# Performance work log

Measured on AMD Instinct MI355X. Metric: run time of the kernel, lower is better.

The kernel has to match this reference:

```python
import jax, jax.numpy as jnp
import numpy as np

N, D, K, A, BINS, DEPTH = 1024, 384, 64, 5, 64, 4
D_MAX = 22.0


def _expected_distance(distogram):
    # distance_one_hot_inverse(softmax(distogram), 0.0, 22.0, 64)
    step = D_MAX / BINS
    centers = step * jnp.arange(BINS, dtype=distogram.dtype) + step / 2
    p = jax.nn.softmax(distogram, axis=-1)  # [N,N,BINS]
    return (p * centers).sum(axis=-1)       # [N,N]


def _extract_neighbours(pos, prev_pos, distogram, resi, chain, batch, mask, key):
    inf = jnp.inf
    same_batch = batch[:, None] == batch[None, :]
    same_chain = (chain[:, None] == chain[None, :]) & same_batch
    pair_mask = mask[:, None] & mask[None, :] & same_batch
    # sequence-separation distance (only within a chain), 3.81 A per residue
    seq_d = jnp.where(same_chain,
                      jnp.abs(resi[:, None] - resi[None, :]).astype(jnp.float32) * 3.81,
                      inf)
    md = _expected_distance(distogram)
    d = jnp.minimum(seq_d, jnp.where(md < 8.0, md, inf))
    ca = pos[:, 1]                                   # current CA positions [N,3]
    d = jnp.minimum(d, jnp.linalg.norm(ca[:, None] - ca[None, :], axis=-1))
    pca = prev_pos[:, 1]
    d = jnp.minimum(d, jnp.linalg.norm(pca[:, None] - pca[None, :], axis=-1))
    d = jnp.where(same_batch, d, inf)
    log_p = -3.0 * d
    u = jax.random.uniform(key, d.shape)
    gumbel = -jnp.log(-jnp.log(u + 1e-6) + 1e-6)
    random_distance = -(log_p + gumbel)
    random_distance = jnp.where(pair_mask, random_distance, inf)
    neg_vals, idx = jax.lax.top_k(-random_distance, K)  # k smallest random distances
    nbr_mask = jnp.isfinite(neg_vals)                   # invalid neighbours have -inf
    return idx, nbr_mask                                # [N,K] int32, [N,K] bool


def setup_inputs() -> dict:
    key = jax.random.key(0)
    ks = jax.random.split(key, 8)
    local = jax.random.normal(ks[0], (N, D), dtype=jnp.float32)
    pos = 3.0 * jax.random.normal(ks[1], (N, A, 3), dtype=jnp.float32)
    prev_pos = 3.0 * jax.random.normal(ks[2], (N, A, 3), dtype=jnp.float32)
    distogram = jax.random.normal(ks[3], (N, N, BINS), dtype=jnp.float32)
    Wn = jax.random.normal(ks[4], (D, D), dtype=jnp.float32) / np.sqrt(D)
    Wp = 0.01 * jax.random.normal(ks[5], (D, A * 3), dtype=jnp.float32)
    ar = jnp.arange(N, dtype=jnp.int32)
    batch = ar // 256          # 4 proteins of 256 residues
    chain = (ar // 128) % 2    # 2 chains per protein
    resi = ar % 128            # residue index within chain
    mask = jnp.ones((N,), dtype=bool)
    return {"local": local, "pos": pos, "prev_pos": prev_pos, "distogram": distogram,
            "Wn": Wn, "Wp": Wp, "resi": resi, "chain": chain, "batch": batch, "mask": mask}


def reference(local, pos, prev_pos, distogram, Wn, Wp, resi, chain, batch, mask):
    mask_f = mask.astype(local.dtype)
    key = jax.random.key(42)
    traj = []
    for t in range(DEPTH):  # diffusion_depth iterations, neighbours recomputed each block
        idx, nbr_mask = _extract_neighbours(pos, prev_pos, distogram, resi, chain,
                                            batch, mask, jax.random.fold_in(key, t))
        nf = local[idx] * nbr_mask[..., None].astype(local.dtype)   # [N,K,D]
        cnt = jnp.maximum(nbr_mask.sum(axis=1, keepdims=True).astype(local.dtype), 1.0)
        msg = nf.sum(axis=1) / cnt                                   # [N,D]
        local = local + jax.nn.gelu(msg @ Wn)
        pos = pos + 0.1 * (local @ Wp).reshape(N, A, 3) * mask_f[:, None, None]
        traj.append(pos)
    trajectory = jnp.stack(traj)  # [DEPTH,N,A,3]
    return local, pos, trajectory
```

## Files before the change

### kernel.cpp

```cpp
#include <hip/hip_runtime.h>
#include <stdint.h>

typedef unsigned int u32;
typedef unsigned long long u64;

#define NN 1024
#define DDIM 384
#define KNB 64
#define BINS_ 64
#define DEPTH_ 4

#define OUT_POS 393216
#define OUT_TRAJ 408576

__device__ __forceinline__ u32 rotl32(u32 x, int r) { return (x << r) | (x >> (32 - r)); }

__device__ __forceinline__ void threefry(u32 k0, u32 k1, u32 x0, u32 x1, u32& o0, u32& o1) {
  u32 ks2 = k0 ^ k1 ^ 0x1BD11BDAu;
#define TF_R(r) { x0 += x1; x1 = rotl32(x1, r); x1 ^= x0; }
  x0 += k0; x1 += k1;
  TF_R(13) TF_R(15) TF_R(26) TF_R(6)
  x0 += k1; x1 += ks2 + 1u;
  TF_R(17) TF_R(29) TF_R(16) TF_R(24)
  x0 += ks2; x1 += k0 + 2u;
  TF_R(13) TF_R(15) TF_R(26) TF_R(6)
  x0 += k0; x1 += k1 + 3u;
  TF_R(17) TF_R(29) TF_R(16) TF_R(24)
  x0 += k1; x1 += ks2 + 4u;
  TF_R(13) TF_R(15) TF_R(26) TF_R(6)
  x0 += ks2; x1 += k0 + 5u;
#undef TF_R
  o0 = x0; o1 = x1;
}

static inline u32 h_rotl32(u32 x, int r) { return (x << r) | (x >> (32 - r)); }
static void h_threefry(u32 k0, u32 k1, u32 x0, u32 x1, u32& o0, u32& o1) {
  u32 ks2 = k0 ^ k1 ^ 0x1BD11BDAu;
#define TF_R(r) { x0 += x1; x1 = h_rotl32(x1, r); x1 ^= x0; }
  x0 += k0; x1 += k1;
  TF_R(13) TF_R(15) TF_R(26) TF_R(6)
  x0 += k1; x1 += ks2 + 1u;
  TF_R(17) TF_R(29) TF_R(16) TF_R(24)
  x0 += ks2; x1 += k0 + 2u;
  TF_R(13) TF_R(15) TF_R(26) TF_R(6)
  x0 += k0; x1 += k1 + 3u;
  TF_R(17) TF_R(29) TF_R(16) TF_R(24)
  x0 += k1; x1 += ks2 + 4u;
  TF_R(13) TF_R(15) TF_R(26) TF_R(6)
  x0 += ks2; x1 += k0 + 5u;
#undef TF_R
  o0 = x0; o1 = x1;
}

__global__ __launch_bounds__(256) void k_dstatic(
    const float* __restrict__ disto, const float* __restrict__ ppos,
    const int* __restrict__ resi, const int* __restrict__ chain,
    const int* __restrict__ batch, float* __restrict__ dstat) {
  int p = blockIdx.x * 256 + threadIdx.x;
  int i = p >> 10, j = p & 1023;
  if (batch[i] != batch[j]) { dstat[p] = __builtin_inff(); return; }
  float seq_d = __builtin_inff();
  if (chain[i] == chain[j]) {
    int dr = resi[i] - resi[j];
    seq_d = __fmul_rn(fabsf((float)dr), 3.81f);
  }
  const float4* dp = reinterpret_cast<const float4*>(disto + (size_t)p * BINS_);
  float w[BINS_];
#pragma unroll
  for (int q = 0; q < 16; ++q) {
    float4 v = dp[q];
    w[4*q+0] = v.x; w[4*q+1] = v.y; w[4*q+2] = v.z; w[4*q+3] = v.w;
  }
  float m = -__builtin_inff();
#pragma unroll
  for (int q = 0; q < BINS_; ++q) m = fmaxf(m, w[q]);
  float s = 0.f;
#pragma unroll
  for (int q = 0; q < BINS_; ++q) {
    w[q] = expf(__fsub_rn(w[q], m));
    s = __fadd_rn(s, w[q]);
  }
  float e = 0.f;
#pragma unroll
  for (int q = 0; q < BINS_; ++q) {
    float pq = __fdiv_rn(w[q], s);
    e = __fadd_rn(e, __fmul_rn(pq, 0.34375f * (float)q + 0.171875f));
  }
  float md = e;
  float d = fminf(seq_d, (md < 8.0f) ? md : __builtin_inff());
  float ax = __fsub_rn(ppos[i*15+3], ppos[j*15+3]);
  float ay = __fsub_rn(ppos[i*15+4], ppos[j*15+4]);
  float az = __fsub_rn(ppos[i*15+5], ppos[j*15+5]);
  float ss = __fadd_rn(__fadd_rn(__fmul_rn(ax,ax), __fmul_rn(ay,ay)), __fmul_rn(az,az));
  dstat[p] = fminf(d, __fsqrt_rn(ss));
}

__device__ __forceinline__ u64 shx64(u64 x, int m) {
  int lo = __shfl_xor((int)(u32)x, m, 64);
  int hi = __shfl_xor((int)(u32)(x >> 32), m, 64);
  return ((u64)(u32)hi << 32) | (u32)lo;
}

__device__ __forceinline__ u64 sort64(u64 x, int lane) {
  for (int size = 2; size <= 64; size <<= 1) {
    for (int stride = size >> 1; stride > 0; stride >>= 1) {
      bool keepmin = (((lane & stride) == 0) == ((lane & size) == 0));
      u64 p = shx64(x, stride);
      u64 lo = (x < p) ? x : p;
      u64 hi = (x < p) ? p : x;
      x = keepmin ? lo : hi;
    }
  }
  return x;
}

__device__ __forceinline__ u64 merge64(u64 a, u64 b, int lane) {
  u64 br = shx64(b, 63);
  u64 m = (a < br) ? a : br;
  for (int stride = 32; stride > 0; stride >>= 1) {
    u64 p = shx64(m, stride);
    u64 lo = (m < p) ? m : p;
    u64 hi = (m < p) ? p : m;
    m = ((lane & stride) == 0) ? lo : hi;
  }
  return m;
}

__global__ __launch_bounds__(64) void k_topk(
    const float* __restrict__ dstat, const float* __restrict__ posP,
    const int* __restrict__ batch, int* __restrict__ idx,
    float* __restrict__ cntv, u32 fk0, u32 fk1) {
  const int i = blockIdx.x;
  const int lane = threadIdx.x;
  const int bi = batch[i];
  const float cax = posP[i*15+3], cay = posP[i*15+4], caz = posP[i*15+5];
  u64 v[16];
  unsigned vmask = 0;
#pragma unroll
  for (int c = 0; c < 16; ++c) {
    int j = c*64 + lane;
    bool sb = (batch[j] == bi);
    if (__ballot(sb) != 0ull) vmask |= (1u << c);
    float rd = __builtin_inff();
    if (sb) {
      float d = dstat[i*NN + j];
      float dx = __fsub_rn(cax, posP[j*15+3]);
      float dy = __fsub_rn(cay, posP[j*15+4]);
      float dz = __fsub_rn(caz, posP[j*15+5]);
      float ss = __fadd_rn(__fadd_rn(__fmul_rn(dx,dx), __fmul_rn(dy,dy)), __fmul_rn(dz,dz));
      d = fminf(d, __fsqrt_rn(ss));
      u32 o0, o1;
      threefry(fk0, fk1, 0u, (u32)(i*NN + j), o0, o1);
      u32 bits = o0 ^ o1;
      float u = __fsub_rn(__uint_as_float((bits >> 9) | 0x3f800000u), 1.0f);
      float inner = __fadd_rn(-logf(__fadd_rn(u, 1e-6f)), 1e-6f);
      float gum = -logf(inner);
      float logp = __fmul_rn(-3.0f, d);
      rd = -__fadd_rn(logp, gum);
    }
    u32 fb = __float_as_uint(rd);
    u32 km = (fb & 0x80000000u) ? ~fb : (fb | 0x80000000u);
    v[c] = ((u64)km << 32) | (u32)j;
  }
#pragma unroll
  for (int c = 0; c < 16; ++c)
    if (vmask & (1u << c)) v[c] = sort64(v[c], lane);
  u64 m1[8]; unsigned vm1 = 0;
#pragma unroll
  for (int c = 0; c < 8; ++c) {
    bool va = (vmask >> (2*c)) & 1u, vb = (vmask >> (2*c+1)) & 1u;
    u64 r = 0;
    if (va && vb) r = merge64(v[2*c], v[2*c+1], lane);
    else if (va) r = v[2*c];
    else if (vb) r = v[2*c+1];
    m1[c] = r; vm1 |= (u32)(va || vb) << c;
  }
  u64 m2[4]; unsigned vm2 = 0;
#pragma unroll
  for (int c = 0; c < 4; ++c) {
    bool va = (vm1 >> (2*c)) & 1u, vb = (vm1 >> (2*c+1)) & 1u;
    u64 r = 0;
    if (va && vb) r = merge64(m1[2*c], m1[2*c+1], lane);
    else if (va) r = m1[2*c];
    else if (vb) r = m1[2*c+1];
    m2[c] = r; vm2 |= (u32)(va || vb) << c;
  }
  u64 m3[2]; unsigned vm3 = 0;
#pragma unroll
  for (int c = 0; c < 2; ++c) {
    bool va = (vm2 >> (2*c)) & 1u, vb = (vm2 >> (2*c+1)) & 1u;
    u64 r = 0;
    if (va && vb) r = merge64(m2[2*c], m2[2*c+1], lane);
    else if (va) r = m2[2*c];
    else if (vb) r = m2[2*c+1];
    m3[c] = r; vm3 |= (u32)(va || vb) << c;
  }
  u64 m;
  {
    bool va = vm3 & 1u, vb = (vm3 >> 1) & 1u;
    if (va && vb) m = merge64(m3[0], m3[1], lane);
    else if (va) m = m3[0];
    else if (vb) m = m3[1];
    else m = ((u64)0xFF800000u << 32) | (u32)lane;
  }
  u32 km = (u32)(m >> 32);
  bool fin = (km < 0xFF800000u);
  idx[i*KNB + lane] = fin ? (int)(u32)(m & 0xffffffffu) : -1;
  u64 ball = __ballot(fin);
  if (lane == 0) cntv[i] = fmaxf((float)__popcll(ball), 1.0f);
}

__global__ __launch_bounds__(384) void k_gmu(
    const float* __restrict__ Lprev, float* __restrict__ Lnext,
    const float* __restrict__ posP, float* __restrict__ posN,
    const int* __restrict__ idx, const float* __restrict__ cntv,
    const float* __restrict__ Wn, const float* __restrict__ Wp,
    float* __restrict__ out, int t) {
  __shared__ int sidx[2][KNB];
  __shared__ float msgT[2][DDIM];
  __shared__ float lrT[2][DDIM + 1];
  const int tid = threadIdx.x;
  const int i0 = blockIdx.x * 2;
  if (tid < 2*KNB) sidx[tid >> 6][tid & 63] = idx[(i0 + (tid >> 6))*KNB + (tid & 63)];
  __syncthreads();
  {
    const int c = tid;
#pragma unroll
    for (int r = 0; r < 2; ++r) {
      float s = 0.f;
#pragma unroll 8
      for (int k = 0; k < KNB; ++k) {
        int id = sidx[r][k];
        if (id >= 0) s += Lprev[id*DDIM + c];
      }
      msgT[r][c] = s / cntv[i0 + r];
    }
  }
  __syncthreads();
  {
    const int c = tid;
    float a0 = 0.f, a1 = 0.f;
#pragma unroll 8
    for (int dd = 0; dd < DDIM; ++dd) {
      float wv = Wn[dd*DDIM + c];
      a0 = fmaf(msgT[0][dd], wv, a0);
      a1 = fmaf(msgT[1][dd], wv, a1);
    }
    float accs[2] = {a0, a1};
#pragma unroll
    for (int r = 0; r < 2; ++r) {
      float x = accs[r];
      float th = tanhf(0.7978845608028654f * (x + 0.044715f * x * x * x));
      float g = 0.5f * x * (1.0f + th);
      float ln = Lprev[(i0 + r)*DDIM + c] + g;
      Lnext[(i0 + r)*DDIM + c] = ln;
      lrT[r][c] = ln;
    }
  }
  __syncthreads();
  if (tid < 30) {
    const int r = tid / 15, cc = tid % 15;
    const int i = i0 + r;
    float acc = 0.f;
#pragma unroll 8
    for (int dd = 0; dd < DDIM; ++dd) acc = fmaf(lrT[r][dd], Wp[dd*15 + cc], acc);
    float pv = posP[i*15 + cc] + 0.1f * acc;
    posN[i*15 + cc] = pv;
    out[OUT_TRAJ + t*15360 + i*15 + cc] = pv;
  }
}

extern "C" void kernel_launch(void* const* d_in, const int* in_sizes, int n_in,
                              void* d_out, int out_size, void* d_ws, size_t ws_size,
                              hipStream_t stream) {
  (void)in_sizes; (void)n_in; (void)out_size; (void)ws_size;
  const float* local_in = (const float*)d_in[0];
  const float* pos_in   = (const float*)d_in[1];
  const float* ppos_in  = (const float*)d_in[2];
  const float* disto    = (const float*)d_in[3];
  const float* Wn       = (const float*)d_in[4];
  const float* Wp       = (const float*)d_in[5];
  const int* resi       = (const int*)d_in[6];
  const int* chain      = (const int*)d_in[7];
  const int* batch      = (const int*)d_in[8];
  float* out = (float*)d_out;
  char* ws = (char*)d_ws;
  float* dstat = (float*)(ws + 0);
  float* L0    = (float*)(ws + 4194304);
  float* L1    = (float*)(ws + 5767168);
  float* P0    = (float*)(ws + 7340032);
  float* P1    = (float*)(ws + 7401472);
  int*   idxb  = (int*)(ws + 7462912);
  float* cntb  = (float*)(ws + 7725056);

  k_dstatic<<<dim3(4096), dim3(256), 0, stream>>>(disto, ppos_in, resi, chain, batch, dstat);

  const float* Lp = local_in;
  const float* Pp = pos_in;
  float* Lbuf[2] = {L0, L1};
  float* Pbuf[2] = {P0, P1};
  for (int t = 0; t < DEPTH_; ++t) {
    u32 fk0, fk1;
    h_threefry(0u, 42u, 0u, (u32)t, fk0, fk1);
    float* Ln = (t == DEPTH_ - 1) ? out : Lbuf[t & 1];
    float* Pn = (t == DEPTH_ - 1) ? (out + OUT_POS) : Pbuf[t & 1];
    k_topk<<<dim3(NN), dim3(64), 0, stream>>>(dstat, Pp, batch, idxb, cntb, fk0, fk1);
    k_gmu<<<dim3(512), dim3(384), 0, stream>>>(Lp, Ln, Pp, Pn, idxb, cntb, Wn, Wp, out, t);
    Lp = Ln; Pp = Pn;
  }
}
```

Measured before the change: 596.0 us.

## Fuse per-round top-k selection into message update kernel and fold softmax expectation

```diff
diff --git a/kernel.cpp b/kernel.cpp
--- a/kernel.cpp
+++ b/kernel.cpp
@@ -74,19 +74,14 @@
   float m = -__builtin_inff();
 #pragma unroll
   for (int q = 0; q < BINS_; ++q) m = fmaxf(m, w[q]);
-  float s = 0.f;
+  float s = 0.f, en = 0.f;
 #pragma unroll
   for (int q = 0; q < BINS_; ++q) {
-    w[q] = expf(__fsub_rn(w[q], m));
-    s = __fadd_rn(s, w[q]);
-  }
-  float e = 0.f;
-#pragma unroll
-  for (int q = 0; q < BINS_; ++q) {
-    float pq = __fdiv_rn(w[q], s);
-    e = __fadd_rn(e, __fmul_rn(pq, 0.34375f * (float)q + 0.171875f));
-  }
-  float md = e;
+    float wq = __expf(__fsub_rn(w[q], m));
+    s = __fadd_rn(s, wq);
+    en = __fadd_rn(en, __fmul_rn(wq, 0.34375f * (float)q + 0.171875f));
+  }
+  float md = __fdiv_rn(en, s);
   float d = fminf(seq_d, (md < 8.0f) ? md : __builtin_inff());
   float ax = __fsub_rn(ppos[i*15+3], ppos[j*15+3]);
   float ay = __fsub_rn(ppos[i*15+4], ppos[j*15+4]);
@@ -126,103 +121,108 @@
   return m;
 }
 
-__global__ __launch_bounds__(64) void k_topk(
-    const float* __restrict__ dstat, const float* __restrict__ posP,
-    const int* __restrict__ batch, int* __restrict__ idx,
-    float* __restrict__ cntv, u32 fk0, u32 fk1) {
-  const int i = blockIdx.x;
-  const int lane = threadIdx.x;
-  const int bi = batch[i];
-  const float cax = posP[i*15+3], cay = posP[i*15+4], caz = posP[i*15+5];
-  u64 v[16];
-  unsigned vmask = 0;
-#pragma unroll
-  for (int c = 0; c < 16; ++c) {
-    int j = c*64 + lane;
-    bool sb = (batch[j] == bi);
-    if (__ballot(sb) != 0ull) vmask |= (1u << c);
-    float rd = __builtin_inff();
-    if (sb) {
-      float d = dstat[i*NN + j];
-      float dx = __fsub_rn(cax, posP[j*15+3]);
-      float dy = __fsub_rn(cay, posP[j*15+4]);
-      float dz = __fsub_rn(caz, posP[j*15+5]);
-      float ss = __fadd_rn(__fadd_rn(__fmul_rn(dx,dx), __fmul_rn(dy,dy)), __fmul_rn(dz,dz));
-      d = fminf(d, __fsqrt_rn(ss));
-      u32 o0, o1;
-      threefry(fk0, fk1, 0u, (u32)(i*NN + j), o0, o1);
-      u32 bits = o0 ^ o1;
-      float u = __fsub_rn(__uint_as_float((bits >> 9) | 0x3f800000u), 1.0f);
-      float inner = __fadd_rn(-logf(__fadd_rn(u, 1e-6f)), 1e-6f);
-      float gum = -logf(inner);
-      float logp = __fmul_rn(-3.0f, d);
-      rd = -__fadd_rn(logp, gum);
-    }
-    u32 fb = __float_as_uint(rd);
-    u32 km = (fb & 0x80000000u) ? ~fb : (fb | 0x80000000u);
-    v[c] = ((u64)km << 32) | (u32)j;
-  }
-#pragma unroll
-  for (int c = 0; c < 16; ++c)
-    if (vmask & (1u << c)) v[c] = sort64(v[c], lane);
-  u64 m1[8]; unsigned vm1 = 0;
-#pragma unroll
-  for (int c = 0; c < 8; ++c) {
-    bool va = (vmask >> (2*c)) & 1u, vb = (vmask >> (2*c+1)) & 1u;
-    u64 r = 0;
-    if (va && vb) r = merge64(v[2*c], v[2*c+1], lane);
-    else if (va) r = v[2*c];
-    else if (vb) r = v[2*c+1];
-    m1[c] = r; vm1 |= (u32)(va || vb) << c;
-  }
-  u64 m2[4]; unsigned vm2 = 0;
-#pragma unroll
-  for (int c = 0; c < 4; ++c) {
-    bool va = (vm1 >> (2*c)) & 1u, vb = (vm1 >> (2*c+1)) & 1u;
-    u64 r = 0;
-    if (va && vb) r = merge64(m1[2*c], m1[2*c+1], lane);
-    else if (va) r = m1[2*c];
-    else if (vb) r = m1[2*c+1];
-    m2[c] = r; vm2 |= (u32)(va || vb) << c;
-  }
-  u64 m3[2]; unsigned vm3 = 0;
-#pragma unroll
-  for (int c = 0; c < 2; ++c) {
-    bool va = (vm2 >> (2*c)) & 1u, vb = (vm2 >> (2*c+1)) & 1u;
-    u64 r = 0;
-    if (va && vb) r = merge64(m2[2*c], m2[2*c+1], lane);
-    else if (va) r = m2[2*c];
-    else if (vb) r = m2[2*c+1];
-    m3[c] = r; vm3 |= (u32)(va || vb) << c;
-  }
-  u64 m;
-  {
-    bool va = vm3 & 1u, vb = (vm3 >> 1) & 1u;
-    if (va && vb) m = merge64(m3[0], m3[1], lane);
-    else if (va) m = m3[0];
-    else if (vb) m = m3[1];
-    else m = ((u64)0xFF800000u << 32) | (u32)lane;
-  }
-  u32 km = (u32)(m >> 32);
-  bool fin = (km < 0xFF800000u);
-  idx[i*KNB + lane] = fin ? (int)(u32)(m & 0xffffffffu) : -1;
-  u64 ball = __ballot(fin);
-  if (lane == 0) cntv[i] = fmaxf((float)__popcll(ball), 1.0f);
-}
-
-__global__ __launch_bounds__(384) void k_gmu(
-    const float* __restrict__ Lprev, float* __restrict__ Lnext,
-    const float* __restrict__ posP, float* __restrict__ posN,
-    const int* __restrict__ idx, const float* __restrict__ cntv,
+__global__ __launch_bounds__(384) void k_round(
+    const float* __restrict__ dstat, const float* __restrict__ Lprev,
+    float* __restrict__ Lnext, const float* __restrict__ posP,
+    float* __restrict__ posN, const int* __restrict__ batch,
     const float* __restrict__ Wn, const float* __restrict__ Wp,
-    float* __restrict__ out, int t) {
+    float* __restrict__ out, int t, u32 fk0, u32 fk1) {
+  __shared__ float sca[NN * 3];
   __shared__ int sidx[2][KNB];
+  __shared__ float scnt[2];
   __shared__ float msgT[2][DDIM];
   __shared__ float lrT[2][DDIM + 1];
   const int tid = threadIdx.x;
+  const int w = tid >> 6, lane = tid & 63;
   const int i0 = blockIdx.x * 2;
-  if (tid < 2*KNB) sidx[tid >> 6][tid & 63] = idx[(i0 + (tid >> 6))*KNB + (tid & 63)];
+
+  for (int e = tid; e < NN * 3; e += 384) {
+    int j = e / 3, k = e - 3 * j;
+    sca[e] = posP[j * 15 + 3 + k];
+  }
   __syncthreads();
+
+  if (w < 2) {
+    const int i = i0 + w;
+    const int bi = batch[i];
+    const float cax = sca[i*3+0], cay = sca[i*3+1], caz = sca[i*3+2];
+    u64 v[16];
+    unsigned vmask = 0;
+#pragma unroll
+    for (int c = 0; c < 16; ++c) {
+      int j = c*64 + lane;
+      bool sb = (batch[j] == bi);
+      if (__ballot(sb) != 0ull) vmask |= (1u << c);
+      float rd = __builtin_inff();
+      if (sb) {
+        float d = dstat[i*NN + j];
+        float dx = __fsub_rn(cax, sca[j*3+0]);
+        float dy = __fsub_rn(cay, sca[j*3+1]);
+        float dz = __fsub_rn(caz, sca[j*3+2]);
+        float ss = __fadd_rn(__fadd_rn(__fmul_rn(dx,dx), __fmul_rn(dy,dy)), __fmul_rn(dz,dz));
+        d = fminf(d, __fsqrt_rn(ss));
+        u32 o0, o1;
+        threefry(fk0, fk1, 0u, (u32)(i*NN + j), o0, o1);
+        u32 bits = o0 ^ o1;
+        float u = __fsub_rn(__uint_as_float((bits >> 9) | 0x3f800000u), 1.0f);
+        float inner = __fadd_rn(-logf(__fadd_rn(u, 1e-6f)), 1e-6f);
+        float gum = -logf(inner);
+        float logp = __fmul_rn(-3.0f, d);
+        rd = -__fadd_rn(logp, gum);
+      }
+      u32 fb = __float_as_uint(rd);
+      u32 km = (fb & 0x80000000u) ? ~fb : (fb | 0x80000000u);
+      v[c] = ((u64)km << 32) | (u32)j;
+    }
+#pragma unroll
+    for (int c = 0; c < 16; ++c)
+      if (vmask & (1u << c)) v[c] = sort64(v[c], lane);
+    u64 m1[8]; unsigned vm1 = 0;
+#pragma unroll
+    for (int c = 0; c < 8; ++c) {
+      bool va = (vmask >> (2*c)) & 1u, vb = (vmask >> (2*c+1)) & 1u;
+      u64 r = 0;
+      if (va && vb) r = merge64(v[2*c], v[2*c+1], lane);
+      else if (va) r = v[2*c];
+      else if (vb) r = v[2*c+1];
+      m1[c] = r; vm1 |= (u32)(va || vb) << c;
+    }
+    u64 m2[4]; unsigned vm2 = 0;
+#pragma unroll
+    for (int c = 0; c < 4; ++c) {
+      bool va = (vm1 >> (2*c)) & 1u, vb = (vm1 >> (2*c+1)) & 1u;
+      u64 r = 0;
+      if (va && vb) r = merge64(m1[2*c], m1[2*c+1], lane);
+      else if (va) r = m1[2*c];
+      else if (vb) r = m1[2*c+1];
+      m2[c] = r; vm2 |= (u32)(va || vb) << c;
+    }
+    u64 m3[2]; unsigned vm3 = 0;
+#pragma unroll
+    for (int c = 0; c < 2; ++c) {
+      bool va = (vm2 >> (2*c)) & 1u, vb = (vm2 >> (2*c+1)) & 1u;
+      u64 r = 0;
+      if (va && vb) r = merge64(m2[2*c], m2[2*c+1], lane);
+      else if (va) r = m2[2*c];
+      else if (vb) r = m2[2*c+1];
+      m3[c] = r; vm3 |= (u32)(va || vb) << c;
+    }
+    u64 m;
+    {
+      bool va = vm3 & 1u, vb = (vm3 >> 1) & 1u;
+      if (va && vb) m = merge64(m3[0], m3[1], lane);
+      else if (va) m = m3[0];
+      else if (vb) m = m3[1];
+      else m = ((u64)0xFF800000u << 32) | (u32)lane;
+    }
+    u32 km = (u32)(m >> 32);
+    bool fin = (km < 0xFF800000u);
+    sidx[w][lane] = fin ? (int)(u32)(m & 0xffffffffu) : -1;
+    u64 ball = __ballot(fin);
+    if (lane == 0) scnt[w] = fmaxf((float)__popcll(ball), 1.0f);
+  }
+  __syncthreads();
+
   {
     const int c = tid;
 #pragma unroll
@@ -233,10 +233,11 @@
         int id = sidx[r][k];
         if (id >= 0) s += Lprev[id*DDIM + c];
       }
-      msgT[r][c] = s / cntv[i0 + r];
+      msgT[r][c] = s / scnt[r];
     }
   }
   __syncthreads();
+
   {
     const int c = tid;
     float a0 = 0.f, a1 = 0.f;
@@ -258,6 +259,7 @@
     }
   }
   __syncthreads();
+
   if (tid < 30) {
     const int r = tid / 15, cc = tid % 15;
     const int i = i0 + r;
@@ -290,8 +292,6 @@
   float* L1    = (float*)(ws + 5767168);
   float* P0    = (float*)(ws + 7340032);
   float* P1    = (float*)(ws + 7401472);
-  int*   idxb  = (int*)(ws + 7462912);
-  float* cntb  = (float*)(ws + 7725056);
 
   k_dstatic<<<dim3(4096), dim3(256), 0, stream>>>(disto, ppos_in, resi, chain, batch, dstat);
 
@@ -304,8 +304,8 @@
     h_threefry(0u, 42u, 0u, (u32)t, fk0, fk1);
     float* Ln = (t == DEPTH_ - 1) ? out : Lbuf[t & 1];
     float* Pn = (t == DEPTH_ - 1) ? (out + OUT_POS) : Pbuf[t & 1];
-    k_topk<<<dim3(NN), dim3(64), 0, stream>>>(dstat, Pp, batch, idxb, cntb, fk0, fk1);
-    k_gmu<<<dim3(512), dim3(384), 0, stream>>>(Lp, Ln, Pp, Pn, idxb, cntb, Wn, Wp, out, t);
+    k_round<<<dim3(512), dim3(384), 0, stream>>>(dstat, Lp, Ln, Pp, Pn, batch,
+                                                 Wn, Wp, out, t, fk0, fk1);
     Lp = Ln; Pp = Pn;
   }
 }
```

Measured after the change: 592.0 us. About the same (-0.7%).
